# Optimization experiments

Hardware: AMD Instinct MI355X
Metric: run time of the kernel (lower is better)

## Reference

```python
import jax, jax.numpy as jnp
import numpy as np

BETA = 0.25


def setup_inputs() -> dict:
    key = jax.random.key(0)
    k1, k2 = jax.random.split(key)
    latents = jax.random.normal(k1, (16, 32, 32, 256), dtype=jnp.float32)
    codebook = jax.random.normal(k2, (8192, 256), dtype=jnp.float32) * 0.05
    return {"latents": latents, "codebook": codebook}


def reference(latents, codebook):
    # latents: [B, H, W, D]; codebook: [V, D]
    B, H, W, D = latents.shape
    flat = latents.reshape(-1, D)  # [N, D], N = B*H*W
    dist = (jnp.sum(flat * flat, axis=1, keepdims=True)
            + jnp.sum(codebook * codebook, axis=1)
            - 2.0 * jnp.einsum('nd,vd->nv', flat, codebook))  # [N, V]
    min_encoding_indices = jnp.argmin(dist, axis=1)  # [N]
    quantized = codebook[min_encoding_indices].reshape(B, H, W, D)
    sg = jax.lax.stop_gradient
    codebook_loss = (jnp.mean((sg(quantized) - latents) ** 2)
                     + BETA * jnp.mean((quantized - sg(latents)) ** 2))
    # straight-through estimator
    quantized_st = latents + sg(quantized - latents)
    return quantized_st, codebook_loss, min_encoding_indices
```

## Files before the change

kernel.cpp:

```cpp
#include <hip/hip_runtime.h>

#define N_ROWS 16384
#define DDIM   256
#define VCODES 8192
#define BETA   0.25f

using f16   = _Float16;
using f16x4 = __attribute__((ext_vector_type(4))) _Float16;
using f16x8 = __attribute__((ext_vector_type(8))) _Float16;
using f32x4 = __attribute__((ext_vector_type(4))) float;

typedef __attribute__((address_space(1))) const unsigned int gu32_t;
typedef __attribute__((address_space(3))) unsigned int       lu32_t;

__device__ __forceinline__ void gload16(const void* g, void* l) {
    __builtin_amdgcn_global_load_lds((gu32_t*)g, (lu32_t*)l, 16, 0, 0);
}

__global__ void split_lat(const float* __restrict__ lat, f16* __restrict__ Ah) {
    int t = blockIdx.x * 256 + threadIdx.x;
    float4 x = *(const float4*)&lat[(size_t)t * 4];
    int row = t >> 6;
    int col = (t & 63) * 4;
    f16 h0 = (f16)x.x, h1 = (f16)x.y, h2 = (f16)x.z, h3 = (f16)x.w;
    f16 l0 = (f16)(x.x - (float)h0), l1 = (f16)(x.y - (float)h1);
    f16 l2 = (f16)(x.z - (float)h2), l3 = (f16)(x.w - (float)h3);
    f16x4 hi = {h0, h1, h2, h3}, lo = {l0, l1, l2, l3};
    *(f16x4*)&Ah[(size_t)row * 512 + col]       = hi;
    *(f16x4*)&Ah[(size_t)row * 512 + 256 + col] = lo;
}

__global__ void split_cb(const float* __restrict__ cb, f16* __restrict__ Bh) {
    int t = blockIdx.x * 256 + threadIdx.x;
    float4 e = *(const float4*)&cb[(size_t)t * 4];
    float ex = e.x * 64.0f, ey = e.y * 64.0f, ez = e.z * 64.0f, ew = e.w * 64.0f;
    int row = t >> 6;
    int col = (t & 63) * 4;
    f16 h0 = (f16)ex, h1 = (f16)ey, h2 = (f16)ez, h3 = (f16)ew;
    f16 l0 = (f16)(ex - (float)h0), l1 = (f16)(ey - (float)h1);
    f16 l2 = (f16)(ez - (float)h2), l3 = (f16)(ew - (float)h3);
    f16x4 hi = {h0, h1, h2, h3}, lo = {l0, l1, l2, l3};
    *(f16x4*)&Bh[(size_t)row * 512 + col]       = hi;
    *(f16x4*)&Bh[(size_t)row * 512 + 256 + col] = lo;
}

__global__ void cbnorm_k(const float* __restrict__ cb, float* __restrict__ cbnorm) {
    int gtid = blockIdx.x * blockDim.x + threadIdx.x;
    int wave = gtid >> 6;
    int lane = threadIdx.x & 63;
    if (wave >= VCODES) return;
    float4 v = *(const float4*)(cb + (size_t)wave * DDIM + lane * 4);
    float s = v.x * v.x + v.y * v.y + v.z * v.z + v.w * v.w;
    #pragma unroll
    for (int m = 32; m; m >>= 1) s += __shfl_xor(s, m, 64);
    if (lane == 0) cbnorm[wave] = s;
}

__global__ __launch_bounds__(256, 2)
void vq_mfma(const f16* __restrict__ Ah, const f16* __restrict__ Bh,
             const float* __restrict__ cbn,
             float* __restrict__ pmin, int* __restrict__ pidx) {
    __shared__ __align__(16) f16 As[128 * 32];
    __shared__ __align__(16) f16 Bs[128 * 32];

    const int tid  = threadIdx.x;
    const int lane = tid & 63;
    const int w    = tid >> 6;
    const int wr   = w >> 1, wc = w & 1;
    const int l15  = lane & 15;
    const int l4   = lane >> 4;
    const int r0   = blockIdx.x * 128;
    const int vgrp = blockIdx.y;

    float rmin[4][4];
    int   ridx[4][4];
    #pragma unroll
    for (int m = 0; m < 4; m++)
        #pragma unroll
        for (int r = 0; r < 4; r++) { rmin[m][r] = 3.4e38f; ridx[m][r] = 0x7fffffff; }

    for (int vt = 0; vt < 4; vt++) {
        const int v0 = vgrp * 512 + vt * 128;
        f32x4 acc[4][4];
        #pragma unroll
        for (int m = 0; m < 4; m++)
            #pragma unroll
            for (int n = 0; n < 4; n++) acc[m][n] = (f32x4){0.f, 0.f, 0.f, 0.f};

        for (int kc = 0; kc < 768; kc += 32) {
            const int acol = (kc < 256) ? kc : kc - 256;
            const int bcol = (kc < 512) ? kc : kc - 512;
            #pragma unroll
            for (int i = 0; i < 2; i++) {
                const int off  = i * 4096 + tid * 16;
                const int row  = off >> 6;
                const int colh = (off >> 1) & 31;
                gload16(Ah + (((size_t)(r0 + row)) << 9) + acol + colh, (char*)As + off);
                gload16(Bh + (((size_t)(v0 + row)) << 9) + bcol + colh, (char*)Bs + off);
            }
            __syncthreads();

            f16x8 af[4], bf[4];
            #pragma unroll
            for (int m = 0; m < 4; m++)
                af[m] = *(const f16x8*)(As + (wr * 64 + m * 16 + l15) * 32 + l4 * 8);
            #pragma unroll
            for (int n = 0; n < 4; n++)
                bf[n] = *(const f16x8*)(Bs + (wc * 64 + n * 16 + l15) * 32 + l4 * 8);
            #pragma unroll
            for (int m = 0; m < 4; m++)
                #pragma unroll
                for (int n = 0; n < 4; n++)
                    acc[m][n] = __builtin_amdgcn_mfma_f32_16x16x32_f16(af[m], bf[n], acc[m][n], 0, 0, 0);
            __syncthreads();
        }

        #pragma unroll
        for (int n = 0; n < 4; n++) {
            const int c = v0 + wc * 64 + n * 16 + l15;
            const float cn = cbn[c];
            #pragma unroll
            for (int m = 0; m < 4; m++)
                #pragma unroll
                for (int r = 0; r < 4; r++) {
                    float s = cn - acc[m][n][r] * 0.03125f;
                    if (s < rmin[m][r] || (s == rmin[m][r] && c < ridx[m][r])) {
                        rmin[m][r] = s; ridx[m][r] = c;
                    }
                }
        }
    }

    #pragma unroll
    for (int m = 0; m < 4; m++)
        #pragma unroll
        for (int r = 0; r < 4; r++) {
            float mv = rmin[m][r];
            int   id = ridx[m][r];
            #pragma unroll
            for (int o = 1; o < 16; o <<= 1) {
                float om = __shfl_xor(mv, o, 64);
                int  oid = __shfl_xor(id, o, 64);
                if (om < mv || (om == mv && oid < id)) { mv = om; id = oid; }
            }
            if (l15 == 0) {
                const int grow = r0 + wr * 64 + m * 16 + l4 * 4 + r;
                pmin[grow * 32 + vgrp * 2 + wc] = mv;
                pidx[grow * 32 + vgrp * 2 + wc] = id;
            }
        }
}

__global__ void combine_k(const float* __restrict__ lat, const float* __restrict__ cb,
                          const float* __restrict__ pmin, const int* __restrict__ pidx,
                          float* __restrict__ out_q, float* __restrict__ out_idx,
                          float* __restrict__ loss_part) {
    const int tid = threadIdx.x, lane = tid & 63, wv = tid >> 6;
    const int row = blockIdx.x * 4 + wv;

    float m = 3.4e38f; int id = 0x7fffffff;
    if (lane < 32) { m = pmin[row * 32 + lane]; id = pidx[row * 32 + lane]; }
    #pragma unroll
    for (int o = 32; o; o >>= 1) {
        float om = __shfl_xor(m, o, 64);
        int  oid = __shfl_xor(id, o, 64);
        if (om < m || (om == m && oid < id)) { m = om; id = oid; }
    }

    float4 q = *(const float4*)&cb[(size_t)id * DDIM + lane * 4];
    float4 x = *(const float4*)&lat[(size_t)row * DDIM + lane * 4];
    *(float4*)&out_q[(size_t)row * DDIM + lane * 4] = q;
    if (lane == 0) out_idx[row] = (float)id;

    float dx = q.x - x.x, dy = q.y - x.y, dz = q.z - x.z, dw = q.w - x.w;
    float s = dx * dx + dy * dy + dz * dz + dw * dw;
    #pragma unroll
    for (int o = 32; o; o >>= 1) s += __shfl_xor(s, o, 64);

    __shared__ float red[4];
    if (lane == 0) red[wv] = s;
    __syncthreads();
    if (tid == 0) loss_part[blockIdx.x] = red[0] + red[1] + red[2] + red[3];
}

__global__ void loss_k(const float* __restrict__ part, float* __restrict__ out_loss) {
    float s = 0.0f;
    for (int i = threadIdx.x; i < N_ROWS / 4; i += 256) s += part[i];
    #pragma unroll
    for (int m = 32; m; m >>= 1) s += __shfl_xor(s, m, 64);
    __shared__ float wsum[4];
    int lane = threadIdx.x & 63, w = threadIdx.x >> 6;
    if (lane == 0) wsum[w] = s;
    __syncthreads();
    if (threadIdx.x == 0) {
        float t = wsum[0] + wsum[1] + wsum[2] + wsum[3];
        *out_loss = (1.0f + BETA) * t / (float)((size_t)N_ROWS * DDIM);
    }
}

extern "C" void kernel_launch(void* const* d_in, const int* in_sizes, int n_in,
                              void* d_out, int out_size, void* d_ws, size_t ws_size,
                              hipStream_t stream) {
    const float* lat = (const float*)d_in[0];
    const float* cb  = (const float*)d_in[1];

    float* ws = (float*)d_ws;
    f16*   Ah       = (f16*)ws;
    f16*   Bh       = (f16*)(ws + 4194304);
    float* cbn      = ws + 4194304 + 2097152;
    float* pmin     = cbn + VCODES;
    int*   pidx     = (int*)(pmin + N_ROWS * 32);
    float* losspart = (float*)(pidx + N_ROWS * 32);

    float* out_q    = (float*)d_out;
    float* out_loss = out_q + (size_t)N_ROWS * DDIM;
    float* out_idx  = out_loss + 1;

    split_lat<<<N_ROWS * DDIM / 1024, 256, 0, stream>>>(lat, Ah);
    split_cb<<<VCODES * DDIM / 1024, 256, 0, stream>>>(cb, Bh);
    cbnorm_k<<<VCODES / 4, 256, 0, stream>>>(cb, cbn);

    dim3 grid(N_ROWS / 128, VCODES / 512);
    vq_mfma<<<grid, 256, 0, stream>>>(Ah, Bh, cbn, pmin, pidx);

    combine_k<<<N_ROWS / 4, 256, 0, stream>>>(lat, cb, pmin, pidx,
                                              out_q, out_idx, losspart);
    loss_k<<<1, 256, 0, stream>>>(losspart, out_loss);
}
```

Baseline: 301.4 us.

## Pre-pack fp16 operands into MFMA fragment layout and double-buffer LDS K-tiles

```diff
diff --git a/kernel.cpp b/kernel.cpp
--- a/kernel.cpp
+++ b/kernel.cpp
@@ -17,31 +17,38 @@
     __builtin_amdgcn_global_load_lds((gu32_t*)g, (lu32_t*)l, 16, 0, 0);
 }
 
-__global__ void split_lat(const float* __restrict__ lat, f16* __restrict__ Ah) {
+
+__global__ void split_lat(const float* __restrict__ lat, f16* __restrict__ Ap) {
     int t = blockIdx.x * 256 + threadIdx.x;
     float4 x = *(const float4*)&lat[(size_t)t * 4];
     int row = t >> 6;
-    int col = (t & 63) * 4;
+    int c   = (t & 63) * 4;
     f16 h0 = (f16)x.x, h1 = (f16)x.y, h2 = (f16)x.z, h3 = (f16)x.w;
     f16 l0 = (f16)(x.x - (float)h0), l1 = (f16)(x.y - (float)h1);
     f16 l2 = (f16)(x.z - (float)h2), l3 = (f16)(x.w - (float)h3);
     f16x4 hi = {h0, h1, h2, h3}, lo = {l0, l1, l2, l3};
-    *(f16x4*)&Ah[(size_t)row * 512 + col]       = hi;
-    *(f16x4*)&Ah[(size_t)row * 512 + 256 + col] = lo;
-}
-
-__global__ void split_cb(const float* __restrict__ cb, f16* __restrict__ Bh) {
+    int kt  = c >> 5;
+    int sub = ((c & 31) >> 3) * 128 + (row & 15) * 8 + (c & 7);
+    size_t base = ((size_t)(row >> 4) * 16);
+    *(f16x4*)&Ap[(base + kt)     * 512 + sub] = hi;
+    *(f16x4*)&Ap[(base + kt + 8) * 512 + sub] = lo;
+}
+
+__global__ void split_cb(const float* __restrict__ cb, f16* __restrict__ Bp) {
     int t = blockIdx.x * 256 + threadIdx.x;
     float4 e = *(const float4*)&cb[(size_t)t * 4];
     float ex = e.x * 64.0f, ey = e.y * 64.0f, ez = e.z * 64.0f, ew = e.w * 64.0f;
     int row = t >> 6;
-    int col = (t & 63) * 4;
+    int c   = (t & 63) * 4;
     f16 h0 = (f16)ex, h1 = (f16)ey, h2 = (f16)ez, h3 = (f16)ew;
     f16 l0 = (f16)(ex - (float)h0), l1 = (f16)(ey - (float)h1);
     f16 l2 = (f16)(ez - (float)h2), l3 = (f16)(ew - (float)h3);
     f16x4 hi = {h0, h1, h2, h3}, lo = {l0, l1, l2, l3};
-    *(f16x4*)&Bh[(size_t)row * 512 + col]       = hi;
-    *(f16x4*)&Bh[(size_t)row * 512 + 256 + col] = lo;
+    int kt  = c >> 5;
+    int sub = ((c & 31) >> 3) * 128 + (row & 15) * 8 + (c & 7);
+    size_t base = ((size_t)(row >> 4) * 16);
+    *(f16x4*)&Bp[(base + kt)     * 512 + sub] = hi;
+    *(f16x4*)&Bp[(base + kt + 8) * 512 + sub] = lo;
 }
 
 __global__ void cbnorm_k(const float* __restrict__ cb, float* __restrict__ cbnorm) {
@@ -57,11 +64,11 @@
 }
 
 __global__ __launch_bounds__(256, 2)
-void vq_mfma(const f16* __restrict__ Ah, const f16* __restrict__ Bh,
+void vq_mfma(const f16* __restrict__ Ap, const f16* __restrict__ Bp,
              const float* __restrict__ cbn,
              float* __restrict__ pmin, int* __restrict__ pidx) {
-    __shared__ __align__(16) f16 As[128 * 32];
-    __shared__ __align__(16) f16 Bs[128 * 32];
+    __shared__ __align__(16) f16 As[2][16 * 512];
+    __shared__ __align__(16) f16 Bs[2][16 * 512];
 
     const int tid  = threadIdx.x;
     const int lane = tid & 63;
@@ -72,6 +79,31 @@
     const int r0   = blockIdx.x * 128;
     const int vgrp = blockIdx.y;
 
+    const char* Ag = (const char*)Ap + (size_t)(r0 >> 4) * 16384;
+    const char* Bp0 = (const char*)Bp;
+
+    auto stage = [&](int vt_, int vc_, int b) {
+        const int akt = (vc_ < 8) ? (vc_ & 3) * 2 : 8 + (vc_ - 8) * 2;
+        const int bkt = (vc_ < 4) ? vc_ * 2 : (vc_ < 8) ? 8 + (vc_ - 4) * 2 : (vc_ - 8) * 2;
+        const char* Bg = Bp0 + (size_t)((vgrp * 512 + vt_ * 128) >> 4) * 16384;
+        #pragma unroll
+        for (int i = 0; i < 4; i++) {
+            const int off = i * 4096 + tid * 16;
+            const int s   = off >> 11;
+            const int h   = (off >> 10) & 1;
+            const int win = off & 1023;
+            gload16(Ag + ((size_t)s * 16 + (akt + h)) * 1024 + win, (char*)As[b] + off);
+        }
+        #pragma unroll
+        for (int i = 0; i < 4; i++) {
+            const int off = i * 4096 + tid * 16;
+            const int s   = off >> 11;
+            const int h   = (off >> 10) & 1;
+            const int win = off & 1023;
+            gload16(Bg + ((size_t)s * 16 + (bkt + h)) * 1024 + win, (char*)Bs[b] + off);
+        }
+    };
+
     float rmin[4][4];
     int   ridx[4][4];
     #pragma unroll
@@ -79,40 +111,41 @@
         #pragma unroll
         for (int r = 0; r < 4; r++) { rmin[m][r] = 3.4e38f; ridx[m][r] = 0x7fffffff; }
 
+    stage(0, 0, 0);
+
     for (int vt = 0; vt < 4; vt++) {
         const int v0 = vgrp * 512 + vt * 128;
+
         f32x4 acc[4][4];
         #pragma unroll
         for (int m = 0; m < 4; m++)
             #pragma unroll
             for (int n = 0; n < 4; n++) acc[m][n] = (f32x4){0.f, 0.f, 0.f, 0.f};
 
-        for (int kc = 0; kc < 768; kc += 32) {
-            const int acol = (kc < 256) ? kc : kc - 256;
-            const int bcol = (kc < 512) ? kc : kc - 512;
-            #pragma unroll
-            for (int i = 0; i < 2; i++) {
-                const int off  = i * 4096 + tid * 16;
-                const int row  = off >> 6;
-                const int colh = (off >> 1) & 31;
-                gload16(Ah + (((size_t)(r0 + row)) << 9) + acol + colh, (char*)As + off);
-                gload16(Bh + (((size_t)(v0 + row)) << 9) + bcol + colh, (char*)Bs + off);
-            }
+        for (int vc = 0; vc < 12; vc++) {
+            const int cc = vt * 12 + vc;
+            const int b  = cc & 1;
             __syncthreads();
-
-            f16x8 af[4], bf[4];
-            #pragma unroll
-            for (int m = 0; m < 4; m++)
-                af[m] = *(const f16x8*)(As + (wr * 64 + m * 16 + l15) * 32 + l4 * 8);
-            #pragma unroll
-            for (int n = 0; n < 4; n++)
-                bf[n] = *(const f16x8*)(Bs + (wc * 64 + n * 16 + l15) * 32 + l4 * 8);
-            #pragma unroll
-            for (int m = 0; m < 4; m++)
+            if (cc < 47) {
+                const int nvt = (vc == 11) ? vt + 1 : vt;
+                const int nvc = (vc == 11) ? 0 : vc + 1;
+                stage(nvt, nvc, (cc + 1) & 1);
+            }
+            #pragma unroll
+            for (int h = 0; h < 2; h++) {
+                f16x8 af[4], bf[4];
+                #pragma unroll
+                for (int m = 0; m < 4; m++)
+                    af[m] = *(const f16x8*)(As[b] + ((wr * 4 + m) * 2 + h) * 512 + lane * 8);
                 #pragma unroll
                 for (int n = 0; n < 4; n++)
-                    acc[m][n] = __builtin_amdgcn_mfma_f32_16x16x32_f16(af[m], bf[n], acc[m][n], 0, 0, 0);
-            __syncthreads();
+                    bf[n] = *(const f16x8*)(Bs[b] + ((wc * 4 + n) * 2 + h) * 512 + lane * 8);
+                #pragma unroll
+                for (int m = 0; m < 4; m++)
+                    #pragma unroll
+                    for (int n = 0; n < 4; n++)
+                        acc[m][n] = __builtin_amdgcn_mfma_f32_16x16x32_f16(af[m], bf[n], acc[m][n], 0, 0, 0);
+            }
         }
 
         #pragma unroll
@@ -205,8 +238,8 @@
     const float* cb  = (const float*)d_in[1];
 
     float* ws = (float*)d_ws;
-    f16*   Ah       = (f16*)ws;
-    f16*   Bh       = (f16*)(ws + 4194304);
+    f16*   Ap       = (f16*)ws;
+    f16*   Bp       = (f16*)(ws + 4194304);
     float* cbn      = ws + 4194304 + 2097152;
     float* pmin     = cbn + VCODES;
     int*   pidx     = (int*)(pmin + N_ROWS * 32);
@@ -216,12 +249,12 @@
     float* out_loss = out_q + (size_t)N_ROWS * DDIM;
     float* out_idx  = out_loss + 1;
 
-    split_lat<<<N_ROWS * DDIM / 1024, 256, 0, stream>>>(lat, Ah);
-    split_cb<<<VCODES * DDIM / 1024, 256, 0, stream>>>(cb, Bh);
+    split_lat<<<N_ROWS * DDIM / 1024, 256, 0, stream>>>(lat, Ap);
+    split_cb<<<VCODES * DDIM / 1024, 256, 0, stream>>>(cb, Bp);
     cbnorm_k<<<VCODES / 4, 256, 0, stream>>>(cb, cbn);
 
     dim3 grid(N_ROWS / 128, VCODES / 512);
-    vq_mfma<<<grid, 256, 0, stream>>>(Ah, Bh, cbn, pmin, pidx);
+    vq_mfma<<<grid, 256, 0, stream>>>(Ap, Bp, cbn, pmin, pidx);
 
     combine_k<<<N_ROWS / 4, 256, 0, stream>>>(lat, cb, pmin, pidx,
                                               out_q, out_idx, losspart);
```

Measured after the change: 312.9 us. 1.04x slower.
